# Kernel optimization log

Hardware: AMD Instinct MI355X
Metric: run time of the kernel (lower is better)

Reference implementation:

```python
import jax, jax.numpy as jnp
import numpy as np

N_NODES = 100000
N_EDGES = 1600000
IN_F = 48
OUT_F = 48


def setup_inputs() -> dict:
    key = jax.random.key(0)
    k1, k2, k3, k4 = jax.random.split(key, 4)
    x = jax.random.normal(k1, (N_NODES, IN_F), dtype=jnp.float32)
    edge_index = jax.random.randint(k2, (2, N_EDGES), 0, N_NODES, dtype=jnp.int32)
    # nn.Linear(in_features, out_features): W is [out, in], b is [out]
    bound = 1.0 / np.sqrt(IN_F)
    W = jax.random.uniform(k3, (OUT_F, IN_F), minval=-bound, maxval=bound, dtype=jnp.float32)
    b = jax.random.uniform(k4, (OUT_F,), minval=-bound, maxval=bound, dtype=jnp.float32)
    return {"x": x, "edge_index": edge_index, "W": W, "b": b}


def reference(x, edge_index, W, b):
    row, col = edge_index[0], edge_index[1]
    n = x.shape[0]
    # degree of each node as message target (bincount over row)
    deg = jnp.bincount(row, length=n).astype(x.dtype)
    deg_inv_sqrt = jnp.where(deg > 0, jax.lax.rsqrt(jnp.where(deg > 0, deg, 1.0)), 0.0)
    norm = deg_inv_sqrt[row] * deg_inv_sqrt[col]          # [E]
    # symmetric-normalized GCN aggregation: sum over edges of norm * x[col] into row
    msg = norm[:, None] * x[col]                           # [E, in]
    agg = jax.ops.segment_sum(msg, row, num_segments=n)    # [N, in]
    out = agg @ W.T + b                                    # [N, out]
    return jax.nn.relu(out)
```

## Files before the change

### kernel.cpp

```cpp
#include <hip/hip_runtime.h>


#define NF 48
#define NPAIR 24
#define ZLD 32
#define RB 128
#define RSH 25
#define CMASK 0x1ffffffu
#define CHUNK 16384
#define CAP 4096
#define SCOL_CAP 4096
#define NSPLIT 2

typedef __attribute__((ext_vector_type(8))) short frag_ab;
typedef __attribute__((ext_vector_type(4))) float f32x4;

__device__ inline unsigned short f2bf(float f) {
    unsigned u = __float_as_uint(f);
    u = (u + 0x7fffu + ((u >> 16) & 1u)) >> 16;
    return (unsigned short)u;
}

__global__ void histA_kernel(const int* __restrict__ row, int* __restrict__ blkhist,
                             int NBUK, int SL, int E) {
    extern __shared__ int hist[];
    const int b  = blockIdx.x / NSPLIT;
    const int sp = blockIdx.x % NSPLIT;
    const int klo = sp * SL;
    const int khi = min(NBUK, klo + SL);
    for (int i = threadIdx.x; i < SL; i += blockDim.x) hist[i] = 0;
    __syncthreads();
    int s = b * CHUNK, t = min(E, s + CHUNK);
    int nv = (t - s) >> 2;
    const int4* r4 = (const int4*)(row + s);
    for (int i = threadIdx.x; i < nv; i += blockDim.x) {
        int4 r = r4[i];
        int k0 = r.x >> 7; if (k0 >= klo && k0 < khi) atomicAdd(&hist[k0 - klo], 1);
        int k1 = r.y >> 7; if (k1 >= klo && k1 < khi) atomicAdd(&hist[k1 - klo], 1);
        int k2 = r.z >> 7; if (k2 >= klo && k2 < khi) atomicAdd(&hist[k2 - klo], 1);
        int k3 = r.w >> 7; if (k3 >= klo && k3 < khi) atomicAdd(&hist[k3 - klo], 1);
    }
    for (int e = s + nv * 4 + threadIdx.x; e < t; e += blockDim.x) {
        int k0 = row[e] >> 7;
        if (k0 >= klo && k0 < khi) atomicAdd(&hist[k0 - klo], 1);
    }
    __syncthreads();
    int* dst = blkhist + (size_t)b * NBUK;
    for (int k = klo + threadIdx.x; k < khi; k += blockDim.x) dst[k] = hist[k - klo];
}

__global__ void scanB1_kernel(int* __restrict__ blkhist, int* __restrict__ btotal,
                              int NBUK, int NCH) {
    int k = blockIdx.x;
    int lane = threadIdx.x;
    int carry = 0;
    for (int base = 0; base < NCH; base += 64) {
        int i = base + lane;
        int v = (i < NCH) ? blkhist[(size_t)i * NBUK + k] : 0;
        int incl = v;
        #pragma unroll
        for (int off = 1; off < 64; off <<= 1) {
            int u = __shfl_up(incl, off, 64);
            if (lane >= off) incl += u;
        }
        if (i < NCH) blkhist[(size_t)i * NBUK + k] = carry + incl - v;
        carry += __shfl(incl, 63, 64);
    }
    if (lane == 0) btotal[k] = carry;
}

__global__ void scatC_kernel(const int* __restrict__ row, const int* __restrict__ col,
                             const int* __restrict__ blkhist,
                             unsigned* __restrict__ binned, int NBUK, int SL, int E) {
    extern __shared__ int cur[];
    const int b  = blockIdx.x / NSPLIT;
    const int sp = blockIdx.x % NSPLIT;
    const int klo = sp * SL;
    const int khi = min(NBUK, klo + SL);
    const int* boff = blkhist + (size_t)b * NBUK;
    for (int k = klo + threadIdx.x; k < khi; k += blockDim.x)
        cur[k - klo] = k * CAP + boff[k];
    __syncthreads();
    int s = b * CHUNK, t = min(E, s + CHUNK);
    int nv = (t - s) >> 2;
    const int4* r4 = (const int4*)(row + s);
    const int4* c4 = (const int4*)(col + s);
    for (int i = threadIdx.x; i < nv; i += blockDim.x) {
        int4 r = r4[i];
        int4 c = c4[i];
        int k0 = r.x >> 7;
        if (k0 >= klo && k0 < khi) {
            int p = atomicAdd(&cur[k0 - klo], 1);
            if (p < (k0 + 1) * CAP)
                binned[p] = ((unsigned)(r.x & (RB - 1)) << RSH) | (unsigned)c.x;
        }
        int k1 = r.y >> 7;
        if (k1 >= klo && k1 < khi) {
            int p = atomicAdd(&cur[k1 - klo], 1);
            if (p < (k1 + 1) * CAP)
                binned[p] = ((unsigned)(r.y & (RB - 1)) << RSH) | (unsigned)c.y;
        }
        int k2 = r.z >> 7;
        if (k2 >= klo && k2 < khi) {
            int p = atomicAdd(&cur[k2 - klo], 1);
            if (p < (k2 + 1) * CAP)
                binned[p] = ((unsigned)(r.z & (RB - 1)) << RSH) | (unsigned)c.z;
        }
        int k3 = r.w >> 7;
        if (k3 >= klo && k3 < khi) {
            int p = atomicAdd(&cur[k3 - klo], 1);
            if (p < (k3 + 1) * CAP)
                binned[p] = ((unsigned)(r.w & (RB - 1)) << RSH) | (unsigned)c.w;
        }
    }
    for (int e = s + nv * 4 + threadIdx.x; e < t; e += blockDim.x) {
        int r = row[e], c = col[e];
        int k0 = r >> 7;
        if (k0 >= klo && k0 < khi) {
            int p = atomicAdd(&cur[k0 - klo], 1);
            if (p < (k0 + 1) * CAP)
                binned[p] = ((unsigned)(r & (RB - 1)) << RSH) | (unsigned)c;
        }
    }
}

__global__ __launch_bounds__(512)
void distrans_kernel(const int* __restrict__ btotal, const unsigned* __restrict__ binned,
                     const float* __restrict__ x, const float* __restrict__ W,
                     float* __restrict__ dis, int* __restrict__ lrp_g,
                     unsigned short* __restrict__ zp16, int N) {
    __shared__ int hist[RB];
    __shared__ float disS[RB];
    __shared__ unsigned short Xb[RB * 64];
    __shared__ unsigned short Wb[48 * 64];
    const int b = blockIdx.x;
    const int tid = threadIdx.x;
    const int nb0 = b * RB;
    const int s = b * CAP;
    const int t = s + min(btotal[b], CAP);

    if (tid < RB) hist[tid] = 0;
    __syncthreads();
    for (int e = s + tid; e < t; e += 512)
        atomicAdd(&hist[binned[e] >> RSH], 1);

    const float4* x4 = (const float4*)x;
    for (int i = tid; i < RB * 12; i += 512) {
        int r = i / 12, c = i % 12;
        int n = nb0 + r;
        float4 v = (n < N) ? x4[(size_t)n * 12 + c] : make_float4(0.f, 0.f, 0.f, 0.f);
        unsigned short* d = &Xb[r * 64 + c * 4];
        d[0] = f2bf(v.x); d[1] = f2bf(v.y); d[2] = f2bf(v.z); d[3] = f2bf(v.w);
    }
    for (int i = tid; i < RB * 8; i += 512)
        ((unsigned*)Xb)[(i >> 3) * 32 + 24 + (i & 7)] = 0u;
    const float4* W4 = (const float4*)W;
    for (int i = tid; i < 576; i += 512) {
        int r = i / 12, c = i % 12;
        float4 v = W4[r * 12 + c];
        unsigned short* d = &Wb[r * 64 + c * 4];
        d[0] = f2bf(v.x); d[1] = f2bf(v.y); d[2] = f2bf(v.z); d[3] = f2bf(v.w);
    }
    for (int i = tid; i < 48 * 8; i += 512)
        ((unsigned*)Wb)[(i >> 3) * 32 + 24 + (i & 7)] = 0u;
    __syncthreads();

    if (tid < 64) {
        int* lp = lrp_g + (size_t)b * (RB + 1);
        int carry = 0;
        for (int base = 0; base < RB; base += 64) {
            int i = base + tid;
            int v = hist[i];
            int incl = v;
            #pragma unroll
            for (int off = 1; off < 64; off <<= 1) {
                int u = __shfl_up(incl, off, 64);
                if (tid >= off) incl += u;
            }
            lp[i] = carry + incl - v;
            float dv = (v > 0) ? rsqrtf((float)v) : 0.0f;
            disS[i] = dv;
            int n = nb0 + i;
            if (n < N) dis[n] = dv;
            carry += __shfl(incl, 63, 64);
        }
        if (tid == 0) lp[RB] = carry;
    }
    __syncthreads();

    const int wv = tid >> 6, lane = tid & 63;
    const int quad = lane >> 4, l16 = lane & 15;
    const int mrow = wv * 16 + l16;

    frag_ab A0 = *(const frag_ab*)&Xb[mrow * 64 + quad * 8];
    frag_ab A1 = *(const frag_ab*)&Xb[mrow * 64 + 32 + quad * 8];
    f32x4 acc[3];
#pragma unroll
    for (int tt = 0; tt < 3; tt++) {
        frag_ab B0 = *(const frag_ab*)&Wb[(tt * 16 + l16) * 64 + quad * 8];
        frag_ab B1 = *(const frag_ab*)&Wb[(tt * 16 + l16) * 64 + 32 + quad * 8];
        f32x4 z = {0.f, 0.f, 0.f, 0.f};
        z = __builtin_amdgcn_mfma_f32_16x16x32_bf16(A0, B0, z, 0, 0, 0);
        z = __builtin_amdgcn_mfma_f32_16x16x32_bf16(A1, B1, z, 0, 0, 0);
        acc[tt] = z;
    }
#pragma unroll
    for (int r = 0; r < 4; r++) {
        int lrow = wv * 16 + quad * 4 + r;
        int n = nb0 + lrow;
        if (n < N) {
            float dn = disS[lrow];
            unsigned short* zr = zp16 + (size_t)n * (2 * ZLD);
#pragma unroll
            for (int tt = 0; tt < 3; tt++)
                zr[tt * 16 + l16] = f2bf(dn * acc[tt][r]);
            zr[48 + l16] = 0;
        }
    }
}

#define GATHER4(KV, KE, A0, A1)                                             \
    {                                                                       \
        int k1_ = (KV) + 2, k2_ = (KV) + 4, k3_ = (KV) + 6;                 \
        bool v1_ = k1_ < (KE), v2_ = k2_ < (KE), v3_ = k3_ < (KE);          \
        int c0_ = scol[(KV)];                                               \
        int c1_ = scol[v1_ ? k1_ : (KV)];                                   \
        int c2_ = scol[v2_ ? k2_ : (KV)];                                   \
        int c3_ = scol[v3_ ? k3_ : (KV)];                                   \
        unsigned u0_ = zp[(size_t)c0_ + ja];                                \
        unsigned u1_ = zp[(size_t)c1_ + ja];                                \
        unsigned u2_ = zp[(size_t)c2_ + ja];                                \
        unsigned u3_ = zp[(size_t)c3_ + ja];                                \
        float f00_ = __uint_as_float(u0_ << 16);                            \
        float f01_ = v1_ ? __uint_as_float(u1_ << 16) : 0.0f;               \
        float f02_ = v2_ ? __uint_as_float(u2_ << 16) : 0.0f;               \
        float f03_ = v3_ ? __uint_as_float(u3_ << 16) : 0.0f;               \
        (A0) += (f00_ + f01_) + (f02_ + f03_);                              \
        float f10_ = __uint_as_float(u0_ & 0xffff0000u);                    \
        float f11_ = v1_ ? __uint_as_float(u1_ & 0xffff0000u) : 0.0f;       \
        float f12_ = v2_ ? __uint_as_float(u2_ & 0xffff0000u) : 0.0f;       \
        float f13_ = v3_ ? __uint_as_float(u3_ & 0xffff0000u) : 0.0f;       \
        (A1) += (f10_ + f11_) + (f12_ + f13_);                              \
    }

__global__ __launch_bounds__(512, 8)
void aggregate_kernel(const int* __restrict__ btotal, const unsigned* __restrict__ binned,
                      const int* __restrict__ lrp_g,
                      const unsigned* __restrict__ zp, const float* __restrict__ dis,
                      const float* __restrict__ bias, float* __restrict__ out, int N) {
    __shared__ int scol[SCOL_CAP];
    __shared__ int lrp[RB + 1];
    __shared__ int cur[RB];
    const int b = blockIdx.x;
    const int s = b * CAP;
    const int cnt = btotal[b];
    const int t = s + min(cnt, CAP);
    const int tid = threadIdx.x;
    if (tid < RB + 1) {
        int v = lrp_g[(size_t)b * (RB + 1) + tid];
        lrp[tid] = v;
        if (tid < RB) cur[tid] = v;
    }
    __syncthreads();
    const bool sorted = (cnt <= SCOL_CAP);
    if (sorted) {
        for (int e = s + tid; e < t; e += 512) {
            unsigned rc = binned[e];
            int pos = atomicAdd(&cur[rc >> RSH], 1);
            scol[pos] = (int)((rc & CMASK) << 5);
        }
    }
    __syncthreads();

    const int lane = tid & 63;
    const int wave = tid >> 6;
    const int h = lane >> 5;
    const int j = lane & 31;
    const bool act = (j < NPAIR);
    const int ja = act ? j : 0;
    float bb0 = 0.0f, bb1 = 0.0f;
    if (act) { bb0 = bias[2 * j]; bb1 = bias[2 * j + 1]; }
    const int rbase = b * RB;
    for (int ri = wave; ri < RB; ri += 16) {
        const int riA = ri, riB = ri + 8;
        const int rA = rbase + riA, rB = rbase + riB;
        float a0A = 0.0f, a1A = 0.0f, a0B = 0.0f, a1B = 0.0f;
        if (sorted) {
            int keA = lrp[riA + 1], keB = lrp[riB + 1];
            int kA = lrp[riA] + h, kB = lrp[riB] + h;
            while (kA < keA && kB < keB) {
                GATHER4(kA, keA, a0A, a1A)
                GATHER4(kB, keB, a0B, a1B)
                kA += 8; kB += 8;
            }
            for (; kA < keA; kA += 8) GATHER4(kA, keA, a0A, a1A)
            for (; kB < keB; kB += 8) GATHER4(kB, keB, a0B, a1B)
        } else {
            for (int e = s; e < t; e++) {
                unsigned rc = binned[e];
                int rr = (int)(rc >> RSH);
                if (h == 0 && act && (rr == riA || rr == riB)) {
                    unsigned u0 = zp[((size_t)(rc & CMASK) << 5) + ja];
                    if (rr == riA) {
                        a0A += __uint_as_float(u0 << 16);
                        a1A += __uint_as_float(u0 & 0xffff0000u);
                    } else {
                        a0B += __uint_as_float(u0 << 16);
                        a1B += __uint_as_float(u0 & 0xffff0000u);
                    }
                }
            }
        }
        a0A += __shfl_xor(a0A, 32, 64);
        a1A += __shfl_xor(a1A, 32, 64);
        a0B += __shfl_xor(a0B, 32, 64);
        a1B += __shfl_xor(a1B, 32, 64);
        if (h == 0 && act) {
            if (rA < N) {
                float dr = dis[rA];
                float v0 = dr * a0A + bb0;
                float v1 = dr * a1A + bb1;
                float2 o;
                o.x = v0 > 0.0f ? v0 : 0.0f;
                o.y = v1 > 0.0f ? v1 : 0.0f;
                *(float2*)(out + (size_t)rA * NF + 2 * j) = o;
            }
            if (rB < N) {
                float dr = dis[rB];
                float v0 = dr * a0B + bb0;
                float v1 = dr * a1B + bb1;
                float2 o;
                o.x = v0 > 0.0f ? v0 : 0.0f;
                o.y = v1 > 0.0f ? v1 : 0.0f;
                *(float2*)(out + (size_t)rB * NF + 2 * j) = o;
            }
        }
    }
}

extern "C" void kernel_launch(void* const* d_in, const int* in_sizes, int n_in,
                              void* d_out, int out_size, void* d_ws, size_t ws_size,
                              hipStream_t stream) {
    const float* x    = (const float*)d_in[0];
    const int*   ei   = (const int*)d_in[1];
    const float* W    = (const float*)d_in[2];
    const float* bias = (const float*)d_in[3];
    float* out = (float*)d_out;

    const int N = in_sizes[0] / NF;
    const int E = in_sizes[1] / 2;
    const int* row = ei;
    const int* col = ei + E;
    const int NBUK = (N + RB - 1) / RB;
    const int NCH  = (E + CHUNK - 1) / CHUNK;
    const int SL   = (NBUK + NSPLIT - 1) / NSPLIT;

    char* ws = (char*)d_ws;
    unsigned* zp      = (unsigned*)ws;       ws += (size_t)N * ZLD * 4;
    unsigned* binned  = (unsigned*)ws;       ws += (size_t)NBUK * CAP * 4;
    float*    dis     = (float*)ws;          ws += (size_t)N * 4;
    int*      blkhist = (int*)ws;            ws += (size_t)NCH * NBUK * 4;
    int*      btotal  = (int*)ws;            ws += (size_t)NBUK * 4;
    int*      lrp_g   = (int*)ws;            ws += (size_t)NBUK * (RB + 1) * 4;

    histA_kernel<<<NCH * NSPLIT, 512, SL * 4, stream>>>(row, blkhist, NBUK, SL, E);
    scanB1_kernel<<<NBUK, 64, 0, stream>>>(blkhist, btotal, NBUK, NCH);
    scatC_kernel<<<NCH * NSPLIT, 512, SL * 4, stream>>>(row, col, blkhist, binned,
                                                        NBUK, SL, E);
    distrans_kernel<<<NBUK, 512, 0, stream>>>(btotal, binned, x, W, dis, lrp_g,
                                              (unsigned short*)zp, N);
    aggregate_kernel<<<NBUK, 512, 0, stream>>>(btotal, binned, lrp_g, zp, dis, bias, out, N);
}
```

Measured before the change: 145.3 us.

## Use persistent blocks with atomic work queue for distrans and aggregate kernels

Both the transform and aggregate kernels now launch a fixed grid of persistent blocks. Each block pulls bucket indices from a global atomic counter, and the counters are reset in the scan kernel. This amortizes per-block setup such as the W bf16 conversion and is meant to improve load balance across uneven buckets. The cost is an extra atomic and barrier per bucket, plus possible hazards where shared memory is reused across loop iterations without a trailing barrier.

```diff
diff --git a/kernel.cpp b/kernel.cpp
--- a/kernel.cpp
+++ b/kernel.cpp
@@ -11,6 +11,7 @@
 #define CAP 4096
 #define SCOL_CAP 4096
 #define NSPLIT 2
+#define PGRID 1024
 
 typedef __attribute__((ext_vector_type(8))) short frag_ab;
 typedef __attribute__((ext_vector_type(4))) float f32x4;
@@ -50,7 +51,8 @@
 }
 
 __global__ void scanB1_kernel(int* __restrict__ blkhist, int* __restrict__ btotal,
-                              int NBUK, int NCH) {
+                              int* __restrict__ wq, int NBUK, int NCH) {
+    if (blockIdx.x == 0 && threadIdx.x == 0) { wq[0] = 0; wq[1] = 0; }
     int k = blockIdx.x;
     int lane = threadIdx.x;
     int carry = 0;
@@ -128,32 +130,15 @@
 void distrans_kernel(const int* __restrict__ btotal, const unsigned* __restrict__ binned,
                      const float* __restrict__ x, const float* __restrict__ W,
                      float* __restrict__ dis, int* __restrict__ lrp_g,
-                     unsigned short* __restrict__ zp16, int N) {
+                     unsigned short* __restrict__ zp16, int* __restrict__ wq,
+                     int NBUK, int N) {
+    __shared__ int sb;
     __shared__ int hist[RB];
     __shared__ float disS[RB];
     __shared__ unsigned short Xb[RB * 64];
     __shared__ unsigned short Wb[48 * 64];
-    const int b = blockIdx.x;
     const int tid = threadIdx.x;
-    const int nb0 = b * RB;
-    const int s = b * CAP;
-    const int t = s + min(btotal[b], CAP);
-
-    if (tid < RB) hist[tid] = 0;
-    __syncthreads();
-    for (int e = s + tid; e < t; e += 512)
-        atomicAdd(&hist[binned[e] >> RSH], 1);
-
-    const float4* x4 = (const float4*)x;
-    for (int i = tid; i < RB * 12; i += 512) {
-        int r = i / 12, c = i % 12;
-        int n = nb0 + r;
-        float4 v = (n < N) ? x4[(size_t)n * 12 + c] : make_float4(0.f, 0.f, 0.f, 0.f);
-        unsigned short* d = &Xb[r * 64 + c * 4];
-        d[0] = f2bf(v.x); d[1] = f2bf(v.y); d[2] = f2bf(v.z); d[3] = f2bf(v.w);
-    }
-    for (int i = tid; i < RB * 8; i += 512)
-        ((unsigned*)Xb)[(i >> 3) * 32 + 24 + (i & 7)] = 0u;
+
     const float4* W4 = (const float4*)W;
     for (int i = tid; i < 576; i += 512) {
         int r = i / 12, c = i % 12;
@@ -163,58 +148,84 @@
     }
     for (int i = tid; i < 48 * 8; i += 512)
         ((unsigned*)Wb)[(i >> 3) * 32 + 24 + (i & 7)] = 0u;
-    __syncthreads();
-
-    if (tid < 64) {
-        int* lp = lrp_g + (size_t)b * (RB + 1);
-        int carry = 0;
-        for (int base = 0; base < RB; base += 64) {
-            int i = base + tid;
-            int v = hist[i];
-            int incl = v;
-            #pragma unroll
-            for (int off = 1; off < 64; off <<= 1) {
-                int u = __shfl_up(incl, off, 64);
-                if (tid >= off) incl += u;
-            }
-            lp[i] = carry + incl - v;
-            float dv = (v > 0) ? rsqrtf((float)v) : 0.0f;
-            disS[i] = dv;
-            int n = nb0 + i;
-            if (n < N) dis[n] = dv;
-            carry += __shfl(incl, 63, 64);
-        }
-        if (tid == 0) lp[RB] = carry;
-    }
-    __syncthreads();
-
-    const int wv = tid >> 6, lane = tid & 63;
-    const int quad = lane >> 4, l16 = lane & 15;
-    const int mrow = wv * 16 + l16;
-
-    frag_ab A0 = *(const frag_ab*)&Xb[mrow * 64 + quad * 8];
-    frag_ab A1 = *(const frag_ab*)&Xb[mrow * 64 + 32 + quad * 8];
-    f32x4 acc[3];
+
+    const float4* x4 = (const float4*)x;
+    for (;;) {
+        if (tid == 0) sb = atomicAdd(&wq[0], 1);
+        __syncthreads();
+        const int b = sb;
+        if (b >= NBUK) return;
+        const int nb0 = b * RB;
+        const int s = b * CAP;
+        const int t = s + min(btotal[b], CAP);
+
+        if (tid < RB) hist[tid] = 0;
+        __syncthreads();
+        for (int e = s + tid; e < t; e += 512)
+            atomicAdd(&hist[binned[e] >> RSH], 1);
+
+        for (int i = tid; i < RB * 12; i += 512) {
+            int r = i / 12, c = i % 12;
+            int n = nb0 + r;
+            float4 v = (n < N) ? x4[(size_t)n * 12 + c] : make_float4(0.f, 0.f, 0.f, 0.f);
+            unsigned short* d = &Xb[r * 64 + c * 4];
+            d[0] = f2bf(v.x); d[1] = f2bf(v.y); d[2] = f2bf(v.z); d[3] = f2bf(v.w);
+        }
+        for (int i = tid; i < RB * 8; i += 512)
+            ((unsigned*)Xb)[(i >> 3) * 32 + 24 + (i & 7)] = 0u;
+        __syncthreads();
+
+        if (tid < 64) {
+            int* lp = lrp_g + (size_t)b * (RB + 1);
+            int carry = 0;
+            for (int base = 0; base < RB; base += 64) {
+                int i = base + tid;
+                int v = hist[i];
+                int incl = v;
+                #pragma unroll
+                for (int off = 1; off < 64; off <<= 1) {
+                    int u = __shfl_up(incl, off, 64);
+                    if (tid >= off) incl += u;
+                }
+                lp[i] = carry + incl - v;
+                float dv = (v > 0) ? rsqrtf((float)v) : 0.0f;
+                disS[i] = dv;
+                int n = nb0 + i;
+                if (n < N) dis[n] = dv;
+                carry += __shfl(incl, 63, 64);
+            }
+            if (tid == 0) lp[RB] = carry;
+        }
+        __syncthreads();
+
+        const int wv = tid >> 6, lane = tid & 63;
+        const int quad = lane >> 4, l16 = lane & 15;
+        const int mrow = wv * 16 + l16;
+
+        frag_ab A0 = *(const frag_ab*)&Xb[mrow * 64 + quad * 8];
+        frag_ab A1 = *(const frag_ab*)&Xb[mrow * 64 + 32 + quad * 8];
+        f32x4 acc[3];
 #pragma unroll
-    for (int tt = 0; tt < 3; tt++) {
-        frag_ab B0 = *(const frag_ab*)&Wb[(tt * 16 + l16) * 64 + quad * 8];
-        frag_ab B1 = *(const frag_ab*)&Wb[(tt * 16 + l16) * 64 + 32 + quad * 8];
-        f32x4 z = {0.f, 0.f, 0.f, 0.f};
-        z = __builtin_amdgcn_mfma_f32_16x16x32_bf16(A0, B0, z, 0, 0, 0);
-        z = __builtin_amdgcn_mfma_f32_16x16x32_bf16(A1, B1, z, 0, 0, 0);
-        acc[tt] = z;
-    }
+        for (int tt = 0; tt < 3; tt++) {
+            frag_ab B0 = *(const frag_ab*)&Wb[(tt * 16 + l16) * 64 + quad * 8];
+            frag_ab B1 = *(const frag_ab*)&Wb[(tt * 16 + l16) * 64 + 32 + quad * 8];
+            f32x4 z = {0.f, 0.f, 0.f, 0.f};
+            z = __builtin_amdgcn_mfma_f32_16x16x32_bf16(A0, B0, z, 0, 0, 0);
+            z = __builtin_amdgcn_mfma_f32_16x16x32_bf16(A1, B1, z, 0, 0, 0);
+            acc[tt] = z;
+        }
 #pragma unroll
-    for (int r = 0; r < 4; r++) {
-        int lrow = wv * 16 + quad * 4 + r;
-        int n = nb0 + lrow;
-        if (n < N) {
-            float dn = disS[lrow];
-            unsigned short* zr = zp16 + (size_t)n * (2 * ZLD);
+        for (int r = 0; r < 4; r++) {
+            int lrow = wv * 16 + quad * 4 + r;
+            int n = nb0 + lrow;
+            if (n < N) {
+                float dn = disS[lrow];
+                unsigned short* zr = zp16 + (size_t)n * (2 * ZLD);
 #pragma unroll
-            for (int tt = 0; tt < 3; tt++)
-                zr[tt * 16 + l16] = f2bf(dn * acc[tt][r]);
-            zr[48 + l16] = 0;
+                for (int tt = 0; tt < 3; tt++)
+                    zr[tt * 16 + l16] = f2bf(dn * acc[tt][r]);
+                zr[48 + l16] = 0;
+            }
         }
     }
 }
@@ -247,31 +258,13 @@
 void aggregate_kernel(const int* __restrict__ btotal, const unsigned* __restrict__ binned,
                       const int* __restrict__ lrp_g,
                       const unsigned* __restrict__ zp, const float* __restrict__ dis,
-                      const float* __restrict__ bias, float* __restrict__ out, int N) {
+                      const float* __restrict__ bias, float* __restrict__ out,
+                      int* __restrict__ wq, int NBUK, int N) {
+    __shared__ int sb;
     __shared__ int scol[SCOL_CAP];
     __shared__ int lrp[RB + 1];
     __shared__ int cur[RB];
-    const int b = blockIdx.x;
-    const int s = b * CAP;
-    const int cnt = btotal[b];
-    const int t = s + min(cnt, CAP);
     const int tid = threadIdx.x;
-    if (tid < RB + 1) {
-        int v = lrp_g[(size_t)b * (RB + 1) + tid];
-        lrp[tid] = v;
-        if (tid < RB) cur[tid] = v;
-    }
-    __syncthreads();
-    const bool sorted = (cnt <= SCOL_CAP);
-    if (sorted) {
-        for (int e = s + tid; e < t; e += 512) {
-            unsigned rc = binned[e];
-            int pos = atomicAdd(&cur[rc >> RSH], 1);
-            scol[pos] = (int)((rc & CMASK) << 5);
-        }
-    }
-    __syncthreads();
-
     const int lane = tid & 63;
     const int wave = tid >> 6;
     const int h = lane >> 5;
@@ -280,59 +273,85 @@
     const int ja = act ? j : 0;
     float bb0 = 0.0f, bb1 = 0.0f;
     if (act) { bb0 = bias[2 * j]; bb1 = bias[2 * j + 1]; }
-    const int rbase = b * RB;
-    for (int ri = wave; ri < RB; ri += 16) {
-        const int riA = ri, riB = ri + 8;
-        const int rA = rbase + riA, rB = rbase + riB;
-        float a0A = 0.0f, a1A = 0.0f, a0B = 0.0f, a1B = 0.0f;
+
+    for (;;) {
+        if (tid == 0) sb = atomicAdd(&wq[1], 1);
+        __syncthreads();
+        const int b = sb;
+        if (b >= NBUK) return;
+        const int s = b * CAP;
+        const int cnt = btotal[b];
+        const int t = s + min(cnt, CAP);
+        if (tid < RB + 1) {
+            int v = lrp_g[(size_t)b * (RB + 1) + tid];
+            lrp[tid] = v;
+            if (tid < RB) cur[tid] = v;
+        }
+        __syncthreads();
+        const bool sorted = (cnt <= SCOL_CAP);
         if (sorted) {
-            int keA = lrp[riA + 1], keB = lrp[riB + 1];
-            int kA = lrp[riA] + h, kB = lrp[riB] + h;
-            while (kA < keA && kB < keB) {
-                GATHER4(kA, keA, a0A, a1A)
-                GATHER4(kB, keB, a0B, a1B)
-                kA += 8; kB += 8;
-            }
-            for (; kA < keA; kA += 8) GATHER4(kA, keA, a0A, a1A)
-            for (; kB < keB; kB += 8) GATHER4(kB, keB, a0B, a1B)
-        } else {
-            for (int e = s; e < t; e++) {
+            for (int e = s + tid; e < t; e += 512) {
                 unsigned rc = binned[e];
-                int rr = (int)(rc >> RSH);
-                if (h == 0 && act && (rr == riA || rr == riB)) {
-                    unsigned u0 = zp[((size_t)(rc & CMASK) << 5) + ja];
-                    if (rr == riA) {
-                        a0A += __uint_as_float(u0 << 16);
-                        a1A += __uint_as_float(u0 & 0xffff0000u);
-                    } else {
-                        a0B += __uint_as_float(u0 << 16);
-                        a1B += __uint_as_float(u0 & 0xffff0000u);
+                int pos = atomicAdd(&cur[rc >> RSH], 1);
+                scol[pos] = (int)((rc & CMASK) << 5);
+            }
+        }
+        __syncthreads();
+
+        const int rbase = b * RB;
+        for (int ri = wave; ri < RB; ri += 16) {
+            const int riA = ri, riB = ri + 8;
+            const int rA = rbase + riA, rB = rbase + riB;
+            float a0A = 0.0f, a1A = 0.0f, a0B = 0.0f, a1B = 0.0f;
+            if (sorted) {
+                int keA = lrp[riA + 1], keB = lrp[riB + 1];
+                int kA = lrp[riA] + h, kB = lrp[riB] + h;
+                while (kA < keA && kB < keB) {
+                    GATHER4(kA, keA, a0A, a1A)
+                    GATHER4(kB, keB, a0B, a1B)
+                    kA += 8; kB += 8;
+                }
+                for (; kA < keA; kA += 8) GATHER4(kA, keA, a0A, a1A)
+                for (; kB < keB; kB += 8) GATHER4(kB, keB, a0B, a1B)
+            } else {
+                for (int e = s; e < t; e++) {
+                    unsigned rc = binned[e];
+                    int rr = (int)(rc >> RSH);
+                    if (h == 0 && act && (rr == riA || rr == riB)) {
+                        unsigned u0 = zp[((size_t)(rc & CMASK) << 5) + ja];
+                        if (rr == riA) {
+                            a0A += __uint_as_float(u0 << 16);
+                            a1A += __uint_as_float(u0 & 0xffff0000u);
+                        } else {
+                            a0B += __uint_as_float(u0 << 16);
+                            a1B += __uint_as_float(u0 & 0xffff0000u);
+                        }
                     }
                 }
             }
-        }
-        a0A += __shfl_xor(a0A, 32, 64);
-        a1A += __shfl_xor(a1A, 32, 64);
-        a0B += __shfl_xor(a0B, 32, 64);
-        a1B += __shfl_xor(a1B, 32, 64);
-        if (h == 0 && act) {
-            if (rA < N) {
-                float dr = dis[rA];
-                float v0 = dr * a0A + bb0;
-                float v1 = dr * a1A + bb1;
-                float2 o;
-                o.x = v0 > 0.0f ? v0 : 0.0f;
-                o.y = v1 > 0.0f ? v1 : 0.0f;
-                *(float2*)(out + (size_t)rA * NF + 2 * j) = o;
-            }
-            if (rB < N) {
-                float dr = dis[rB];
-                float v0 = dr * a0B + bb0;
-                float v1 = dr * a1B + bb1;
-                float2 o;
-                o.x = v0 > 0.0f ? v0 : 0.0f;
-                o.y = v1 > 0.0f ? v1 : 0.0f;
-                *(float2*)(out + (size_t)rB * NF + 2 * j) = o;
+            a0A += __shfl_xor(a0A, 32, 64);
+            a1A += __shfl_xor(a1A, 32, 64);
+            a0B += __shfl_xor(a0B, 32, 64);
+            a1B += __shfl_xor(a1B, 32, 64);
+            if (h == 0 && act) {
+                if (rA < N) {
+                    float dr = dis[rA];
+                    float v0 = dr * a0A + bb0;
+                    float v1 = dr * a1A + bb1;
+                    float2 o;
+                    o.x = v0 > 0.0f ? v0 : 0.0f;
+                    o.y = v1 > 0.0f ? v1 : 0.0f;
+                    *(float2*)(out + (size_t)rA * NF + 2 * j) = o;
+                }
+                if (rB < N) {
+                    float dr = dis[rB];
+                    float v0 = dr * a0B + bb0;
+                    float v1 = dr * a1B + bb1;
+                    float2 o;
+                    o.x = v0 > 0.0f ? v0 : 0.0f;
+                    o.y = v1 > 0.0f ? v1 : 0.0f;
+                    *(float2*)(out + (size_t)rB * NF + 2 * j) = o;
+                }
             }
         }
     }
@@ -362,12 +381,14 @@
     int*      blkhist = (int*)ws;            ws += (size_t)NCH * NBUK * 4;
     int*      btotal  = (int*)ws;            ws += (size_t)NBUK * 4;
     int*      lrp_g   = (int*)ws;            ws += (size_t)NBUK * (RB + 1) * 4;
+    int*      wq      = (int*)ws;            ws += 2 * 4;
 
     histA_kernel<<<NCH * NSPLIT, 512, SL * 4, stream>>>(row, blkhist, NBUK, SL, E);
-    scanB1_kernel<<<NBUK, 64, 0, stream>>>(blkhist, btotal, NBUK, NCH);
+    scanB1_kernel<<<NBUK, 64, 0, stream>>>(blkhist, btotal, wq, NBUK, NCH);
     scatC_kernel<<<NCH * NSPLIT, 512, SL * 4, stream>>>(row, col, blkhist, binned,
                                                         NBUK, SL, E);
-    distrans_kernel<<<NBUK, 512, 0, stream>>>(btotal, binned, x, W, dis, lrp_g,
-                                              (unsigned short*)zp, N);
-    aggregate_kernel<<<NBUK, 512, 0, stream>>>(btotal, binned, lrp_g, zp, dis, bias, out, N);
-}
+    distrans_kernel<<<PGRID, 512, 0, stream>>>(btotal, binned, x, W, dis, lrp_g,
+                                               (unsigned short*)zp, wq, NBUK, N);
+    aggregate_kernel<<<PGRID, 512, 0, stream>>>(btotal, binned, lrp_g, zp, dis, bias,
+                                                out, wq, NBUK, N);
+}
```

Measured after the change: 171.7 us. +18.2%, slower.
